# Performance work log

Measured on AMD Instinct MI355X. Metric: run time of the kernel, lower is better.

Reference implementation:

```python
import jax, jax.numpy as jnp
import numpy as np

C, N, D, DQ, K = 8, 16384, 1024, 128, 128  # clusters, patches/cluster, feat dim, q dim, top_k per cluster


def setup_inputs() -> dict:
    key = jax.random.key(0)
    ks = jax.random.split(key, 4)
    s = 0.02
    return {
        "cluster_features": jax.random.normal(ks[0], (C, N, D), jnp.float32),
        "key_feats": jax.random.normal(ks[1], (C, 1, D), jnp.float32),
        "Wq": jax.random.normal(ks[2], (D, DQ), jnp.float32) * s,
        "bq": jnp.zeros((DQ,), jnp.float32),
        "Wv": jax.random.normal(ks[3], (D, D), jnp.float32) * s,
        "bv": jnp.zeros((D,), jnp.float32),
    }


def _ranking_topk(feats, key_feat, Wq, bq, Wv, bv):
    # feats: [n, d], key_feat: [1, d]
    Q = feats @ Wq + bq                     # [n, DQ]
    qk = key_feat @ Wq + bq                 # [1, DQ]
    A = Q @ qk.T                            # [n, 1] attention scores
    A = jax.nn.softmax(A / jnp.sqrt(jnp.float32(DQ)), axis=0)
    top_vals, top_idx = jax.lax.top_k(A[:, 0], K)   # sorted descending, like torch.topk
    top_feats = feats[top_idx]              # [K, d] gather
    V = top_feats @ Wv + bv                 # value projection on gathered subset only
    A_ = jax.nn.softmax(top_vals[:, None] / jnp.sqrt(jnp.float32(D)), axis=0)  # [K, 1]
    fusion = (A_.T @ V)[0]                  # [d] fused weighted sum
    return top_feats, fusion


def reference(cluster_features, key_feats, Wq, bq, Wv, bv):
    top_feats, fusion = jax.vmap(
        lambda f, kf: _ranking_topk(f, kf, Wq, bq, Wv, bv)
    )(cluster_features, key_feats)
    # concat per-cluster selections; C*K == num_sample_feature so no padding branch
    selected_features = top_feats.reshape(C * K, D)
    cluster_fusion_feature = fusion         # [C, D]
    return selected_features, cluster_fusion_feature
```

## Files before the change

kernel.cpp:

```cpp
#include <hip/hip_runtime.h>

#define C_CLUST 8
#define N_PAT   16384
#define D_FEAT  1024
#define DQ_DIM  128
#define K_TOP   128
#define NCHUNK  32
#define CHROWS  512

#define INV_S128 0.08838834764831844055
#define INV_S1024 0.03125

__device__ inline unsigned f2key(float f) {
    unsigned u = __float_as_uint(f);
    return (u & 0x80000000u) ? ~u : (u | 0x80000000u);
}
__device__ inline float key2f(unsigned k) {
    unsigned u = (k & 0x80000000u) ? (k ^ 0x80000000u) : ~k;
    return __uint_as_float(u);
}

__global__ __launch_bounds__(1024) void scoreall_kernel(
    const float* __restrict__ feats,
    const float* __restrict__ key_feats,
    const float* __restrict__ Wq,
    const float* __restrict__ bq,
    unsigned long long* __restrict__ cand,
    unsigned* __restrict__ mxkey,
    double* __restrict__ Ssum)
{
    const int b = blockIdx.x;
    const int c = b >> 5, chunk = b & 31;
    const int tid = threadIdx.x;
    const int lane = tid & 63, wv = tid >> 6;

    __shared__ float keyrow[D_FEAT];
    __shared__ double part[1024];
    __shared__ double qk_lds[DQ_DIM];
    __shared__ double r_lds[D_FEAT];
    __shared__ double b0_lds;
    __shared__ unsigned ured[8];
    __shared__ double dred[8];
    __shared__ unsigned bmax_s;
    __shared__ __align__(16) char ubuf[32768];
    float* wq_tile  = (float*)ubuf;
    float* scores_s = (float*)ubuf;
    unsigned long long* su = (unsigned long long*)(ubuf + 2048);

    keyrow[tid] = key_feats[c * D_FEAT + tid];
    __syncthreads();

    {
        const int j = tid & 127, s = tid >> 7;
        double acc = 0.0;
        for (int d = s; d < D_FEAT; d += 8)
            acc += (double)keyrow[d] * (double)Wq[d * DQ_DIM + j];
        part[s * DQ_DIM + j] = acc;
    }
    __syncthreads();
    if (tid < DQ_DIM) {
        double v = part[tid];
#pragma unroll
        for (int s2 = 1; s2 < 8; ++s2) v += part[s2 * DQ_DIM + tid];
        qk_lds[tid] = v + (double)bq[tid];
    }
    __syncthreads();
    if (wv == 0) {
        double p = (double)bq[lane] * qk_lds[lane] + (double)bq[64 + lane] * qk_lds[64 + lane];
#pragma unroll
        for (int o = 32; o > 0; o >>= 1) p += __shfl_xor(p, o, 64);
        if (lane == 0) b0_lds = p;
    }

    for (int ch = 0; ch < 16; ++ch) {
        __syncthreads();
        {
            const float4* src = (const float4*)(Wq + (size_t)ch * 64 * DQ_DIM);
            float4* dst = (float4*)wq_tile;
            dst[tid * 2 + 0] = src[tid * 2 + 0];
            dst[tid * 2 + 1] = src[tid * 2 + 1];
        }
        __syncthreads();
        const int dloc = tid >> 4, jg = tid & 15;
        double acc = 0.0;
#pragma unroll
        for (int jj = 0; jj < 8; ++jj)
            acc += (double)wq_tile[dloc * DQ_DIM + jg * 8 + jj] * qk_lds[jg * 8 + jj];
        part[dloc * 16 + jg] = acc;
        __syncthreads();
        if (tid < 64) {
            double s = 0.0;
#pragma unroll
            for (int g = 0; g < 16; ++g) s += part[tid * 16 + g];
            r_lds[ch * 64 + tid] = s;
        }
    }
    __syncthreads();

    const double bb = b0_lds;
    double rr[16];
#pragma unroll
    for (int it = 0; it < 4; ++it)
#pragma unroll
        for (int j = 0; j < 4; ++j)
            rr[it * 4 + j] = r_lds[it * 256 + lane * 4 + j];
    const int n0 = chunk * CHROWS + wv * 32;
    const float4* fbase = (const float4*)(feats + (size_t)(c * N_PAT + n0) * D_FEAT);

    for (int rI = 0; rI < 32; rI += 2) {
        const float4* fp0 = fbase + (size_t)(rI + 0) * 256;
        const float4* fp1 = fbase + (size_t)(rI + 1) * 256;
        double acc0 = 0.0, acc1 = 0.0;
#pragma unroll
        for (int it = 0; it < 4; ++it) {
            float4 f0 = fp0[it * 64 + lane];
            float4 f1 = fp1[it * 64 + lane];
            acc0 += (double)f0.x * rr[it * 4 + 0];
            acc0 += (double)f0.y * rr[it * 4 + 1];
            acc0 += (double)f0.z * rr[it * 4 + 2];
            acc0 += (double)f0.w * rr[it * 4 + 3];
            acc1 += (double)f1.x * rr[it * 4 + 0];
            acc1 += (double)f1.y * rr[it * 4 + 1];
            acc1 += (double)f1.z * rr[it * 4 + 2];
            acc1 += (double)f1.w * rr[it * 4 + 3];
        }
#pragma unroll
        for (int o = 32; o > 0; o >>= 1) {
            acc0 += __shfl_xor(acc0, o, 64);
            acc1 += __shfl_xor(acc1, o, 64);
        }
        if (lane == 0) {
            scores_s[wv * 32 + rI + 0] = (float)(acc0 + bb);
            scores_s[wv * 32 + rI + 1] = (float)(acc1 + bb);
        }
    }
    __syncthreads();

    float sc = 0.0f; unsigned key = 0;
    if (tid < CHROWS) { sc = scores_s[tid]; key = f2key(sc); }
    if (tid < CHROWS) {
        unsigned mk = key;
#pragma unroll
        for (int o = 32; o > 0; o >>= 1) mk = max(mk, __shfl_xor(mk, o, 64));
        if (lane == 0) ured[wv] = mk;
    }
    __syncthreads();
    if (tid == 0) {
        unsigned m = ured[0];
        for (int i = 1; i < 8; ++i) m = max(m, ured[i]);
        bmax_s = m;
    }
    __syncthreads();
    const unsigned kmax = bmax_s;
    const double mx_t = (double)key2f(kmax) * INV_S128;
    if (tid < CHROWS) {
        double es = (double)__expf((float)((double)sc * INV_S128 - mx_t));
#pragma unroll
        for (int o = 32; o > 0; o >>= 1) es += __shfl_xor(es, o, 64);
        if (lane == 0) dred[wv] = es;
    }
    __syncthreads();
    if (tid == 0) {
        double z = 0.0;
        for (int i = 0; i < 8; ++i) z += dred[i];
        Ssum[c * NCHUNK + chunk] = z;
        mxkey[c * NCHUNK + chunk] = kmax;
    }
    if (tid < CHROWS)
        su[tid] = ((unsigned long long)key << 32) | (unsigned)(~(unsigned)(chunk * CHROWS + tid));
    for (int k = 2; k <= CHROWS; k <<= 1) {
        for (int j = k >> 1; j > 0; j >>= 1) {
            __syncthreads();
            const int i = tid, l = i ^ j;
            if (i < CHROWS && l > i) {
                unsigned long long a = su[i], b2 = su[l];
                const bool desc = ((i & k) == 0);
                if (desc ? (a < b2) : (a > b2)) { su[i] = b2; su[l] = a; }
            }
        }
    }
    __syncthreads();
    if (tid < K_TOP) cand[(size_t)(c * NCHUNK + chunk) * K_TOP + tid] = su[tid];
}

__global__ __launch_bounds__(1024) void merge_gw_kernel(
    const float* __restrict__ feats,
    const unsigned long long* __restrict__ cand,
    const unsigned* __restrict__ mxkey,
    const double* __restrict__ Ssum,
    float* __restrict__ out,
    double* __restrict__ w)
{
    const int c = blockIdx.x;
    const int tid = threadIdx.x;
    const int lane = tid & 63, wv = tid >> 6;

    __shared__ __align__(16) char mbuf[32768];
    unsigned long long* su2 = (unsigned long long*)mbuf;
    double* wred = (double*)mbuf;
    __shared__ double pd[K_TOP];
    __shared__ double sa[K_TOP];
    __shared__ int sidx[K_TOP];
    __shared__ double dred2[2];
    __shared__ double sZ;

    su2[tid]        = cand[(size_t)c * 4096 + tid];
    su2[tid + 1024] = cand[(size_t)c * 4096 + tid + 1024];
    su2[tid + 2048] = cand[(size_t)c * 4096 + tid + 2048];
    su2[tid + 3072] = cand[(size_t)c * 4096 + tid + 3072];
    __syncthreads();

    for (int nl = 32; nl > 1; nl >>= 1) {
        const int half = nl >> 1;
        const int total = half * K_TOP;
        unsigned long long tmp[2];
        int cnt = 0;
        for (int i = tid; i < total; i += 1024) {
            const int g = i >> 7, li = i & 127;
            unsigned long long a  = su2[(2 * g) * K_TOP + li];
            unsigned long long b2 = su2[(2 * g + 1) * K_TOP + (K_TOP - 1 - li)];
            tmp[cnt++] = a > b2 ? a : b2;
        }
        __syncthreads();
        cnt = 0;
        for (int i = tid; i < total; i += 1024) su2[i] = tmp[cnt++];
        __syncthreads();
        for (int j = 64; j > 0; j >>= 1) {
            for (int i = tid; i < total; i += 1024) {
                const int li = i & 127, l = li ^ j;
                if (l > li) {
                    const int base = i - li;
                    unsigned long long a = su2[base + li], b2 = su2[base + l];
                    if (a < b2) { su2[base + li] = b2; su2[base + l] = a; }
                }
            }
            __syncthreads();
        }
    }

    const double m_t = (double)key2f((unsigned)(su2[0] >> 32)) * INV_S128;
    if (wv == 0) {
        double z = (lane < NCHUNK)
            ? Ssum[c * NCHUNK + lane] * exp((double)key2f(mxkey[c * NCHUNK + lane]) * INV_S128 - m_t)
            : 0.0;
#pragma unroll
        for (int o = 32; o > 0; o >>= 1) z += __shfl_xor(z, o, 64);
        if (lane == 0) sZ = z;
    }
    __syncthreads();
    const double Z = sZ;
    if (tid < K_TOP) {
        unsigned long long pr = su2[tid];
        sidx[tid] = (int)(~(unsigned)(pr & 0xFFFFFFFFull));
        pd[tid] = exp((double)key2f((unsigned)(pr >> 32)) * INV_S128 - m_t) / Z;
    }
    __syncthreads();
    if (tid < K_TOP) {
        double e = exp((pd[tid] - pd[0]) * INV_S1024);
        double se = e;
#pragma unroll
        for (int o = 32; o > 0; o >>= 1) se += __shfl_xor(se, o, 64);
        if (lane == 0) dred2[wv] = se;
    }
    __syncthreads();
    if (tid < K_TOP) {
        double tot = dred2[0] + dred2[1];
        sa[tid] = exp((pd[tid] - pd[0]) * INV_S1024) / tot;
    }
    __syncthreads();

    const int g = tid >> 8, q = tid & 255;
    const float* fc = feats + (size_t)c * N_PAT * D_FEAT;
    float* oc = out + (size_t)c * K_TOP * D_FEAT;
    double a0 = 0.0, a1 = 0.0, a2 = 0.0, a3 = 0.0;
    for (int ig = 0; ig < 32; ++ig) {
        const int i = ig * 4 + g;
        const int row = sidx[i];
        float4 v = ((const float4*)(fc + (size_t)row * D_FEAT))[q];
        ((float4*)(oc + (size_t)i * D_FEAT))[q] = v;
        const double a = sa[i];
        a0 += a * (double)v.x;
        a1 += a * (double)v.y;
        a2 += a * (double)v.z;
        a3 += a * (double)v.w;
    }
    wred[(size_t)(g * 256 + q) * 4 + 0] = a0;
    wred[(size_t)(g * 256 + q) * 4 + 1] = a1;
    wred[(size_t)(g * 256 + q) * 4 + 2] = a2;
    wred[(size_t)(g * 256 + q) * 4 + 3] = a3;
    __syncthreads();
    {
        const int d = tid, q2 = d >> 2, j2 = d & 3;
        double s = wred[(0 * 256 + q2) * 4 + j2] + wred[(1 * 256 + q2) * 4 + j2]
                 + wred[(2 * 256 + q2) * 4 + j2] + wred[(3 * 256 + q2) * 4 + j2];
        w[c * D_FEAT + d] = s;
    }
}

__global__ __launch_bounds__(256) void fusion_kernel(
    const double* __restrict__ w,
    const float* __restrict__ Wv,
    const float* __restrict__ bv,
    float* __restrict__ out)
{
    __shared__ double w_lds[D_FEAT];
    __shared__ double partl[2][128];
    const int b = blockIdx.x;
    const int c = b >> 3, dpg = b & 7;
    const int tid = threadIdx.x;

    for (int d = tid; d < D_FEAT; d += 256) w_lds[d] = w[c * D_FEAT + d];
    __syncthreads();

    const int dpl = tid & 127, half = tid >> 7;
    const int dp = dpg * 128 + dpl;
    const double* wc = w_lds + half * 512;
    const float* wvp = Wv + (size_t)(half * 512) * D_FEAT + dp;
    double a0 = 0.0, a1 = 0.0, a2 = 0.0, a3 = 0.0;
#pragma unroll 2
    for (int d = 0; d < 512; d += 4) {
        a0 += wc[d + 0] * (double)wvp[(size_t)(d + 0) * D_FEAT];
        a1 += wc[d + 1] * (double)wvp[(size_t)(d + 1) * D_FEAT];
        a2 += wc[d + 2] * (double)wvp[(size_t)(d + 2) * D_FEAT];
        a3 += wc[d + 3] * (double)wvp[(size_t)(d + 3) * D_FEAT];
    }
    partl[half][dpl] = (a0 + a1) + (a2 + a3);
    __syncthreads();
    if (half == 0) {
        double acc = (double)bv[dp] + partl[0][dpl] + partl[1][dpl];
        out[(size_t)(C_CLUST * K_TOP * D_FEAT) + c * D_FEAT + dp] = (float)acc;
    }
}

extern "C" void kernel_launch(void* const* d_in, const int* in_sizes, int n_in,
                              void* d_out, int out_size, void* d_ws, size_t ws_size,
                              hipStream_t stream) {
    const float* feats     = (const float*)d_in[0];
    const float* key_feats = (const float*)d_in[1];
    const float* Wq        = (const float*)d_in[2];
    const float* bq        = (const float*)d_in[3];
    const float* Wv        = (const float*)d_in[4];
    const float* bv        = (const float*)d_in[5];
    float* out = (float*)d_out;

    char* ws = (char*)d_ws;
    unsigned long long* cand = (unsigned long long*)(ws + 0);
    double*   Ssum  = (double*)(ws + 262144);
    unsigned* mxkey = (unsigned*)(ws + 264192);
    double*   w     = (double*)(ws + 265216);

    hipLaunchKernelGGL(scoreall_kernel, dim3(256), dim3(1024), 0, stream,
                       feats, key_feats, Wq, bq, cand, mxkey, Ssum);
    hipLaunchKernelGGL(merge_gw_kernel, dim3(C_CLUST), dim3(1024), 0, stream,
                       feats, cand, mxkey, Ssum, out, w);
    hipLaunchKernelGGL(fusion_kernel,   dim3(64), dim3(256), 0, stream,
                       w, Wv, bv, out);
}
```

Baseline: 241.2 us.

## Split scoring into prep, streaming score, chunk-sort and fused tail kernels

The per-cluster projection vector r = Wq·qk is computed once by a separate prep kernel instead of being recomputed redundantly in each of 256 scoring blocks. Scoring becomes a lightweight 256-thread kernel with 2048 blocks that streams features and writes scores to workspace. A separate chunk-sort kernel bitonic-sorts 1024-row chunks. The Wv fusion matvec is folded into the merge kernel, which now runs only 8 blocks, so the extra launches and the score round trip through memory are traded against better parallelism and less duplicated work.

```diff
diff --git a/kernel.cpp b/kernel.cpp
--- a/kernel.cpp
+++ b/kernel.cpp
@@ -5,8 +5,8 @@
 #define D_FEAT  1024
 #define DQ_DIM  128
 #define K_TOP   128
-#define NCHUNK  32
-#define CHROWS  512
+#define NCHUNK  16
+#define CHROWS  1024
 
 #define INV_S128 0.08838834764831844055
 #define INV_S1024 0.03125
@@ -20,32 +20,20 @@
     return __uint_as_float(u);
 }
 
-__global__ __launch_bounds__(1024) void scoreall_kernel(
-    const float* __restrict__ feats,
+__global__ __launch_bounds__(1024) void prep_kernel(
     const float* __restrict__ key_feats,
     const float* __restrict__ Wq,
     const float* __restrict__ bq,
-    unsigned long long* __restrict__ cand,
-    unsigned* __restrict__ mxkey,
-    double* __restrict__ Ssum)
+    double* __restrict__ r,
+    double* __restrict__ b0)
 {
-    const int b = blockIdx.x;
-    const int c = b >> 5, chunk = b & 31;
-    const int tid = threadIdx.x;
-    const int lane = tid & 63, wv = tid >> 6;
-
     __shared__ float keyrow[D_FEAT];
     __shared__ double part[1024];
     __shared__ double qk_lds[DQ_DIM];
-    __shared__ double r_lds[D_FEAT];
-    __shared__ double b0_lds;
-    __shared__ unsigned ured[8];
-    __shared__ double dred[8];
-    __shared__ unsigned bmax_s;
-    __shared__ __align__(16) char ubuf[32768];
-    float* wq_tile  = (float*)ubuf;
-    float* scores_s = (float*)ubuf;
-    unsigned long long* su = (unsigned long long*)(ubuf + 2048);
+    const int b = blockIdx.x;
+    const int c = b >> 3, g = b & 7;
+    const int tid = threadIdx.x;
+    const int lane = tid & 63, wv = tid >> 6;
 
     keyrow[tid] = key_feats[c * D_FEAT + tid];
     __syncthreads();
@@ -65,49 +53,53 @@
         qk_lds[tid] = v + (double)bq[tid];
     }
     __syncthreads();
-    if (wv == 0) {
+
+    if (g == 0 && wv == 0) {
         double p = (double)bq[lane] * qk_lds[lane] + (double)bq[64 + lane] * qk_lds[64 + lane];
 #pragma unroll
         for (int o = 32; o > 0; o >>= 1) p += __shfl_xor(p, o, 64);
-        if (lane == 0) b0_lds = p;
-    }
-
-    for (int ch = 0; ch < 16; ++ch) {
-        __syncthreads();
-        {
-            const float4* src = (const float4*)(Wq + (size_t)ch * 64 * DQ_DIM);
-            float4* dst = (float4*)wq_tile;
-            dst[tid * 2 + 0] = src[tid * 2 + 0];
-            dst[tid * 2 + 1] = src[tid * 2 + 1];
-        }
-        __syncthreads();
-        const int dloc = tid >> 4, jg = tid & 15;
-        double acc = 0.0;
-#pragma unroll
-        for (int jj = 0; jj < 8; ++jj)
-            acc += (double)wq_tile[dloc * DQ_DIM + jg * 8 + jj] * qk_lds[jg * 8 + jj];
-        part[dloc * 16 + jg] = acc;
-        __syncthreads();
-        if (tid < 64) {
-            double s = 0.0;
-#pragma unroll
-            for (int g = 0; g < 16; ++g) s += part[tid * 16 + g];
-            r_lds[ch * 64 + tid] = s;
-        }
-    }
-    __syncthreads();
-
-    const double bb = b0_lds;
+        if (lane == 0) b0[c] = p;
+    }
+
+    {
+        const double q0 = qk_lds[lane], q1 = qk_lds[64 + lane];
+        const int d0 = g * 128 + wv * 8;
+#pragma unroll
+        for (int i = 0; i < 8; ++i) {
+            const int d = d0 + i;
+            double a = (double)Wq[d * DQ_DIM + lane] * q0
+                     + (double)Wq[d * DQ_DIM + 64 + lane] * q1;
+#pragma unroll
+            for (int o = 32; o > 0; o >>= 1) a += __shfl_xor(a, o, 64);
+            if (lane == 0) r[c * D_FEAT + d] = a;
+        }
+    }
+}
+
+__global__ __launch_bounds__(256) void score_kernel(
+    const float* __restrict__ feats,
+    const double* __restrict__ r,
+    const double* __restrict__ b0,
+    float* __restrict__ scores)
+{
+    const int w    = blockIdx.x * 4 + (threadIdx.x >> 6);
+    const int lane = threadIdx.x & 63;
+    const int c  = w >> 10;
+    const int n0 = (w & 1023) * 16;
+
+    const double* rp = r + c * D_FEAT;
     double rr[16];
 #pragma unroll
     for (int it = 0; it < 4; ++it)
 #pragma unroll
         for (int j = 0; j < 4; ++j)
-            rr[it * 4 + j] = r_lds[it * 256 + lane * 4 + j];
-    const int n0 = chunk * CHROWS + wv * 32;
+            rr[it * 4 + j] = rp[it * 256 + lane * 4 + j];
+    const double bb = b0[c];
+
     const float4* fbase = (const float4*)(feats + (size_t)(c * N_PAT + n0) * D_FEAT);
-
-    for (int rI = 0; rI < 32; rI += 2) {
+    float* sout = scores + c * N_PAT + n0;
+
+    for (int rI = 0; rI < 16; rI += 2) {
         const float4* fp0 = fbase + (size_t)(rI + 0) * 256;
         const float4* fp1 = fbase + (size_t)(rI + 1) * 256;
         double acc0 = 0.0, acc1 = 0.0;
@@ -130,49 +122,60 @@
             acc1 += __shfl_xor(acc1, o, 64);
         }
         if (lane == 0) {
-            scores_s[wv * 32 + rI + 0] = (float)(acc0 + bb);
-            scores_s[wv * 32 + rI + 1] = (float)(acc1 + bb);
-        }
-    }
-    __syncthreads();
-
-    float sc = 0.0f; unsigned key = 0;
-    if (tid < CHROWS) { sc = scores_s[tid]; key = f2key(sc); }
-    if (tid < CHROWS) {
-        unsigned mk = key;
-#pragma unroll
-        for (int o = 32; o > 0; o >>= 1) mk = max(mk, __shfl_xor(mk, o, 64));
-        if (lane == 0) ured[wv] = mk;
-    }
+            sout[rI + 0] = (float)(acc0 + bb);
+            sout[rI + 1] = (float)(acc1 + bb);
+        }
+    }
+}
+
+__global__ __launch_bounds__(1024) void chunksort_kernel(
+    const float* __restrict__ scores,
+    unsigned long long* __restrict__ cand,
+    unsigned* __restrict__ mxkey,
+    double* __restrict__ Ssum)
+{
+    const int b = blockIdx.x;
+    const int c = b >> 4, chunk = b & 15;
+    const int tid = threadIdx.x;
+    const int lane = tid & 63, wv = tid >> 6;
+
+    __shared__ unsigned long long su[1024];
+    __shared__ unsigned ured[16];
+    __shared__ double dred[16];
+    __shared__ unsigned bmax_s;
+
+    const float sc = scores[c * N_PAT + chunk * CHROWS + tid];
+    const unsigned key = f2key(sc);
+    unsigned mk = key;
+#pragma unroll
+    for (int o = 32; o > 0; o >>= 1) mk = max(mk, __shfl_xor(mk, o, 64));
+    if (lane == 0) ured[wv] = mk;
     __syncthreads();
     if (tid == 0) {
         unsigned m = ured[0];
-        for (int i = 1; i < 8; ++i) m = max(m, ured[i]);
+        for (int i = 1; i < 16; ++i) m = max(m, ured[i]);
         bmax_s = m;
     }
     __syncthreads();
     const unsigned kmax = bmax_s;
     const double mx_t = (double)key2f(kmax) * INV_S128;
-    if (tid < CHROWS) {
-        double es = (double)__expf((float)((double)sc * INV_S128 - mx_t));
-#pragma unroll
-        for (int o = 32; o > 0; o >>= 1) es += __shfl_xor(es, o, 64);
-        if (lane == 0) dred[wv] = es;
-    }
+    double es = (double)__expf((float)((double)sc * INV_S128 - mx_t));
+#pragma unroll
+    for (int o = 32; o > 0; o >>= 1) es += __shfl_xor(es, o, 64);
+    if (lane == 0) dred[wv] = es;
     __syncthreads();
     if (tid == 0) {
         double z = 0.0;
-        for (int i = 0; i < 8; ++i) z += dred[i];
+        for (int i = 0; i < 16; ++i) z += dred[i];
         Ssum[c * NCHUNK + chunk] = z;
         mxkey[c * NCHUNK + chunk] = kmax;
     }
-    if (tid < CHROWS)
-        su[tid] = ((unsigned long long)key << 32) | (unsigned)(~(unsigned)(chunk * CHROWS + tid));
-    for (int k = 2; k <= CHROWS; k <<= 1) {
+    su[tid] = ((unsigned long long)key << 32) | (unsigned)(~(unsigned)(chunk * CHROWS + tid));
+    for (int k = 2; k <= 1024; k <<= 1) {
         for (int j = k >> 1; j > 0; j >>= 1) {
             __syncthreads();
             const int i = tid, l = i ^ j;
-            if (i < CHROWS && l > i) {
+            if (l > i) {
                 unsigned long long a = su[i], b2 = su[l];
                 const bool desc = ((i & k) == 0);
                 if (desc ? (a < b2) : (a > b2)) { su[i] = b2; su[l] = a; }
@@ -183,13 +186,14 @@
     if (tid < K_TOP) cand[(size_t)(c * NCHUNK + chunk) * K_TOP + tid] = su[tid];
 }
 
-__global__ __launch_bounds__(1024) void merge_gw_kernel(
+__global__ __launch_bounds__(1024) void tail_kernel(
     const float* __restrict__ feats,
     const unsigned long long* __restrict__ cand,
     const unsigned* __restrict__ mxkey,
     const double* __restrict__ Ssum,
-    float* __restrict__ out,
-    double* __restrict__ w)
+    const float* __restrict__ Wv,
+    const float* __restrict__ bv,
+    float* __restrict__ out)
 {
     const int c = blockIdx.x;
     const int tid = threadIdx.x;
@@ -198,19 +202,18 @@
     __shared__ __align__(16) char mbuf[32768];
     unsigned long long* su2 = (unsigned long long*)mbuf;
     double* wred = (double*)mbuf;
+    __shared__ double w_lds[D_FEAT];
     __shared__ double pd[K_TOP];
     __shared__ double sa[K_TOP];
     __shared__ int sidx[K_TOP];
     __shared__ double dred2[2];
     __shared__ double sZ;
 
-    su2[tid]        = cand[(size_t)c * 4096 + tid];
-    su2[tid + 1024] = cand[(size_t)c * 4096 + tid + 1024];
-    su2[tid + 2048] = cand[(size_t)c * 4096 + tid + 2048];
-    su2[tid + 3072] = cand[(size_t)c * 4096 + tid + 3072];
-    __syncthreads();
-
-    for (int nl = 32; nl > 1; nl >>= 1) {
+    su2[tid]        = cand[(size_t)c * 2048 + tid];
+    su2[tid + 1024] = cand[(size_t)c * 2048 + tid + 1024];
+    __syncthreads();
+
+    for (int nl = 16; nl > 1; nl >>= 1) {
         const int half = nl >> 1;
         const int total = half * K_TOP;
         unsigned long long tmp[2];
@@ -291,43 +294,23 @@
     __syncthreads();
     {
         const int d = tid, q2 = d >> 2, j2 = d & 3;
-        double s = wred[(0 * 256 + q2) * 4 + j2] + wred[(1 * 256 + q2) * 4 + j2]
+        w_lds[d] = wred[(0 * 256 + q2) * 4 + j2] + wred[(1 * 256 + q2) * 4 + j2]
                  + wred[(2 * 256 + q2) * 4 + j2] + wred[(3 * 256 + q2) * 4 + j2];
-        w[c * D_FEAT + d] = s;
-    }
-}
-
-__global__ __launch_bounds__(256) void fusion_kernel(
-    const double* __restrict__ w,
-    const float* __restrict__ Wv,
-    const float* __restrict__ bv,
-    float* __restrict__ out)
-{
-    __shared__ double w_lds[D_FEAT];
-    __shared__ double partl[2][128];
-    const int b = blockIdx.x;
-    const int c = b >> 3, dpg = b & 7;
-    const int tid = threadIdx.x;
-
-    for (int d = tid; d < D_FEAT; d += 256) w_lds[d] = w[c * D_FEAT + d];
-    __syncthreads();
-
-    const int dpl = tid & 127, half = tid >> 7;
-    const int dp = dpg * 128 + dpl;
-    const double* wc = w_lds + half * 512;
-    const float* wvp = Wv + (size_t)(half * 512) * D_FEAT + dp;
-    double a0 = 0.0, a1 = 0.0, a2 = 0.0, a3 = 0.0;
+    }
+    __syncthreads();
+
+    {
+        const int dp = tid;
+        const float* wvp = Wv + dp;
+        double f0 = 0.0, f1 = 0.0, f2 = 0.0, f3 = 0.0;
 #pragma unroll 2
-    for (int d = 0; d < 512; d += 4) {
-        a0 += wc[d + 0] * (double)wvp[(size_t)(d + 0) * D_FEAT];
-        a1 += wc[d + 1] * (double)wvp[(size_t)(d + 1) * D_FEAT];
-        a2 += wc[d + 2] * (double)wvp[(size_t)(d + 2) * D_FEAT];
-        a3 += wc[d + 3] * (double)wvp[(size_t)(d + 3) * D_FEAT];
-    }
-    partl[half][dpl] = (a0 + a1) + (a2 + a3);
-    __syncthreads();
-    if (half == 0) {
-        double acc = (double)bv[dp] + partl[0][dpl] + partl[1][dpl];
+        for (int d = 0; d < D_FEAT; d += 4) {
+            f0 += w_lds[d + 0] * (double)wvp[(size_t)(d + 0) * D_FEAT];
+            f1 += w_lds[d + 1] * (double)wvp[(size_t)(d + 1) * D_FEAT];
+            f2 += w_lds[d + 2] * (double)wvp[(size_t)(d + 2) * D_FEAT];
+            f3 += w_lds[d + 3] * (double)wvp[(size_t)(d + 3) * D_FEAT];
+        }
+        double acc = (double)bv[dp] + (f0 + f1) + (f2 + f3);
         out[(size_t)(C_CLUST * K_TOP * D_FEAT) + c * D_FEAT + dp] = (float)acc;
     }
 }
@@ -344,15 +327,19 @@
     float* out = (float*)d_out;
 
     char* ws = (char*)d_ws;
-    unsigned long long* cand = (unsigned long long*)(ws + 0);
-    double*   Ssum  = (double*)(ws + 262144);
-    unsigned* mxkey = (unsigned*)(ws + 264192);
-    double*   w     = (double*)(ws + 265216);
-
-    hipLaunchKernelGGL(scoreall_kernel, dim3(256), dim3(1024), 0, stream,
-                       feats, key_feats, Wq, bq, cand, mxkey, Ssum);
-    hipLaunchKernelGGL(merge_gw_kernel, dim3(C_CLUST), dim3(1024), 0, stream,
-                       feats, cand, mxkey, Ssum, out, w);
-    hipLaunchKernelGGL(fusion_kernel,   dim3(64), dim3(256), 0, stream,
-                       w, Wv, bv, out);
-}
+    float*  scores  = (float*)(ws + 0);
+    double* r       = (double*)(ws + 524288);
+    double* b0      = (double*)(ws + 589824);
+    unsigned long long* cand = (unsigned long long*)(ws + 589888);
+    double*   Ssum  = (double*)(ws + 720960);
+    unsigned* mxkey = (unsigned*)(ws + 721984);
+
+    hipLaunchKernelGGL(prep_kernel,      dim3(64),   dim3(1024), 0, stream,
+                       key_feats, Wq, bq, r, b0);
+    hipLaunchKernelGGL(score_kernel,     dim3(2048), dim3(256),  0, stream,
+                       feats, r, b0, scores);
+    hipLaunchKernelGGL(chunksort_kernel, dim3(128),  dim3(1024), 0, stream,
+                       scores, cand, mxkey, Ssum);
+    hipLaunchKernelGGL(tail_kernel,      dim3(C_CLUST), dim3(1024), 0, stream,
+                       feats, cand, mxkey, Ssum, Wv, bv, out);
+}
```

Result: slower. 263.7 us (+9.3%).
